# Kernel tuning notes

Measured on AMD Instinct MI355X. Metric: run time of the kernel, lower is better.

## Reference

```python
import jax, jax.numpy as jnp
import numpy as np

HID_X = 64
MLP_RATIO = 4
EPS_NORM = 1e-12  # F.normalize default eps
EPS_RMS = 1e-6


def _l2norm_dim2(w):
    # normalize along dim=-2 (the input-feature axis of each per-sample matrix)
    n = jnp.sqrt(jnp.sum(w * w, axis=-2, keepdims=True))
    return w / jnp.maximum(n, EPS_NORM)


def setup_inputs() -> dict:
    key = jax.random.key(0)
    k1, k2, k3, k4 = jax.random.split(key, 4)
    B, N, D, S = 64, 4096, HID_X, 1024
    total = 3 * D * D * MLP_RATIO
    x = jax.random.normal(k1, (B, N, D), dtype=jnp.float32)
    s = jax.random.normal(k2, (B, S), dtype=jnp.float32)
    W_pg = jax.random.normal(k3, (S, total), dtype=jnp.float32) * 0.02
    b_pg = jax.random.normal(k4, (total,), dtype=jnp.float32) * 0.01
    scale = jnp.ones((D,), dtype=jnp.float32)
    return {"x": x, "s": s, "W_pg": W_pg, "b_pg": b_pg, "scale": scale}


def reference(x, s, W_pg, b_pg, scale):
    B, N, D = x.shape
    H = D * MLP_RATIO
    # hypernetwork: generate per-sample MLP weights
    mlp_params = s @ W_pg + b_pg  # [B, 3*D*H]
    g_p, v_p, f_p = jnp.split(mlp_params, 3, axis=-1)
    fc1_gate = _l2norm_dim2(g_p.reshape(B, D, H))
    fc1_value = _l2norm_dim2(v_p.reshape(B, D, H))
    fc2 = _l2norm_dim2(f_p.reshape(B, H, D))
    # RMSNorm (eps=1e-6)
    rrms = jax.lax.rsqrt(jnp.mean(x * x, axis=-1, keepdims=True) + EPS_RMS)
    xn = x * rrms * scale
    gate = jnp.einsum('bnd,bdh->bnh', xn, fc1_gate)
    value = jnp.einsum('bnd,bdh->bnh', xn, fc1_value)
    h = jax.nn.silu(gate) * value
    out = jnp.einsum('bnh,bhd->bnd', h, fc2) + x
    return out
```

## Files before the change

kernel.cpp:

```cpp
#include <hip/hip_runtime.h>
#include <hip/hip_bf16.h>

#define BB 64
#define NN 4096
#define DD 64
#define HH 256
#define SS 1024
#define TOTAL 49152
#define MAT_ELEMS 16384

typedef __bf16 bf16x8 __attribute__((ext_vector_type(8)));
typedef float  f32x4  __attribute__((ext_vector_type(4)));

__global__ __launch_bounds__(256, 4) void k1_gemm(
    const float* __restrict__ s, const float* __restrict__ W,
    const float* __restrict__ bias, float* __restrict__ params)
{
    const int n0 = blockIdx.x * 64;
    const int t  = threadIdx.x;
    const int tx = t & 15, ty = t >> 4;

    __shared__ float sA[64 * 36];
    __shared__ float sB[32 * 68];

    float acc[4][4] = {};

    for (int k0 = 0; k0 < SS; k0 += 32) {
        #pragma unroll
        for (int i = 0; i < 2; i++) {
            int f4i = t + i * 256;
            int m = f4i >> 3, k4 = f4i & 7;
            float4 v = *(const float4*)&s[m * SS + k0 + k4 * 4];
            *(float4*)&sA[m * 36 + k4 * 4] = v;
        }
        #pragma unroll
        for (int i = 0; i < 2; i++) {
            int f4i = t + i * 256;
            int kk = f4i >> 4, n4 = f4i & 15;
            float4 v = *(const float4*)&W[(size_t)(k0 + kk) * TOTAL + n0 + n4 * 4];
            *(float4*)&sB[kk * 68 + n4 * 4] = v;
        }
        __syncthreads();
        #pragma unroll
        for (int kk = 0; kk < 32; kk++) {
            float4 b = *(const float4*)&sB[kk * 68 + tx * 4];
            float a0 = sA[(ty * 4 + 0) * 36 + kk];
            float a1 = sA[(ty * 4 + 1) * 36 + kk];
            float a2 = sA[(ty * 4 + 2) * 36 + kk];
            float a3 = sA[(ty * 4 + 3) * 36 + kk];
            acc[0][0] += a0 * b.x; acc[0][1] += a0 * b.y; acc[0][2] += a0 * b.z; acc[0][3] += a0 * b.w;
            acc[1][0] += a1 * b.x; acc[1][1] += a1 * b.y; acc[1][2] += a1 * b.z; acc[1][3] += a1 * b.w;
            acc[2][0] += a2 * b.x; acc[2][1] += a2 * b.y; acc[2][2] += a2 * b.z; acc[2][3] += a2 * b.w;
            acc[3][0] += a3 * b.x; acc[3][1] += a3 * b.y; acc[3][2] += a3 * b.z; acc[3][3] += a3 * b.w;
        }
        __syncthreads();
    }

    #pragma unroll
    for (int r = 0; r < 4; r++) {
        int m = ty * 4 + r;
        int n = n0 + tx * 4;
        float4 bv = *(const float4*)&bias[n];
        float4 o;
        o.x = acc[r][0] + bv.x; o.y = acc[r][1] + bv.y;
        o.z = acc[r][2] + bv.z; o.w = acc[r][3] + bv.w;
        *(float4*)&params[(size_t)m * TOTAL + n] = o;
    }
}

__global__ __launch_bounds__(256) void k2_fc1(
    const float* __restrict__ params, __bf16* __restrict__ WgT, __bf16* __restrict__ WvT)
{
    const int b   = blockIdx.x >> 2;
    const int mat = (blockIdx.x >> 1) & 1;
    const int hh  = blockIdx.x & 1;
    const int t   = threadIdx.x;
    __shared__ float sh[64 * 130];
    __shared__ float rnorm[128];

    const float* src = params + (size_t)b * TOTAL + mat * MAT_ELEMS + hh * 128;
    #pragma unroll
    for (int i = 0; i < 32; i++) {
        int idx = t + i * 256;
        int d = idx >> 7, h = idx & 127;
        sh[d * 130 + h] = src[d * 256 + h];
    }
    __syncthreads();
    if (t < 128) {
        float sum = 0.f;
        #pragma unroll
        for (int d = 0; d < 64; d++) {
            float v = sh[d * 130 + t];
            sum += v * v;
        }
        rnorm[t] = 1.0f / fmaxf(sqrtf(sum), 1e-12f);
    }
    __syncthreads();
    __bf16* dst = (mat ? WvT : WgT) + (size_t)b * MAT_ELEMS;
    #pragma unroll
    for (int i = 0; i < 32; i++) {
        int idx = t + i * 256;
        int hl = idx >> 6, d = idx & 63;
        dst[(hh * 128 + hl) * 64 + d] = (__bf16)(sh[d * 130 + hl] * rnorm[hl]);
    }
}

__global__ __launch_bounds__(256) void k2_fc2(
    const float* __restrict__ params, __bf16* __restrict__ WfT)
{
    const int b  = blockIdx.x >> 1;
    const int dh = blockIdx.x & 1;
    const int t  = threadIdx.x;
    __shared__ float sh[256 * 33];
    __shared__ float psum[8 * 32];
    __shared__ float rnorm[32];

    const float* src = params + (size_t)b * TOTAL + 2 * MAT_ELEMS + dh * 32;
    #pragma unroll
    for (int i = 0; i < 32; i++) {
        int idx = t + i * 256;
        int h = idx >> 5, d = idx & 31;
        sh[h * 33 + d] = src[h * 64 + d];
    }
    __syncthreads();
    {
        int d = t & 31, seg = t >> 5;
        float sum = 0.f;
        #pragma unroll
        for (int hi = 0; hi < 32; hi++) {
            float v = sh[(seg * 32 + hi) * 33 + d];
            sum += v * v;
        }
        psum[seg * 32 + d] = sum;
    }
    __syncthreads();
    if (t < 32) {
        float sum = 0.f;
        #pragma unroll
        for (int seg = 0; seg < 8; seg++) sum += psum[seg * 32 + t];
        rnorm[t] = 1.0f / fmaxf(sqrtf(sum), 1e-12f);
    }
    __syncthreads();
    __bf16* dst = WfT + (size_t)b * MAT_ELEMS;
    #pragma unroll
    for (int i = 0; i < 32; i++) {
        int idx = t + i * 256;
        int d = idx >> 8, h = idx & 255;
        dst[(dh * 32 + d) * 256 + h] = (__bf16)(sh[h * 33 + d] * rnorm[d]);
    }
}

__global__ __launch_bounds__(256, 4) void k3_fused(
    const float* __restrict__ x, const float* __restrict__ scale,
    const __bf16* __restrict__ WgT, const __bf16* __restrict__ WvT,
    const __bf16* __restrict__ WfT, float* __restrict__ out)
{
    const int b    = blockIdx.x >> 5;
    const int rb   = blockIdx.x & 31;
    const int t    = threadIdx.x;
    const int w    = t >> 6;
    const int lane = t & 63;
    const int l15  = lane & 15;
    const int quad = lane >> 4;

    __shared__ __bf16 h_sh[4 * 32 * 36];

    const size_t row_base = ((size_t)b * NN + rb * 128) * DD;

    float sc[16];
    *(float4*)&sc[0]  = *(const float4*)&scale[quad * 8];
    *(float4*)&sc[4]  = *(const float4*)&scale[quad * 8 + 4];
    *(float4*)&sc[8]  = *(const float4*)&scale[32 + quad * 8];
    *(float4*)&sc[12] = *(const float4*)&scale[32 + quad * 8 + 4];

    bf16x8 afrag[2][2];
    #pragma unroll
    for (int mt = 0; mt < 2; mt++) {
        int row = w * 32 + mt * 16 + l15;
        const float* xp = &x[row_base + (size_t)row * DD + quad * 8];
        float v[16];
        *(float4*)&v[0]  = *(const float4*)(xp);
        *(float4*)&v[4]  = *(const float4*)(xp + 4);
        *(float4*)&v[8]  = *(const float4*)(xp + 32);
        *(float4*)&v[12] = *(const float4*)(xp + 36);
        float ss = 0.f;
        #pragma unroll
        for (int j = 0; j < 16; j++) ss += v[j] * v[j];
        ss += __shfl_xor(ss, 16, 64);
        ss += __shfl_xor(ss, 32, 64);
        float rr = rsqrtf(ss * (1.0f / 64.0f) + 1e-6f);
        #pragma unroll
        for (int j = 0; j < 8; j++) {
            afrag[mt][0][j] = (__bf16)(v[j] * rr * sc[j]);
            afrag[mt][1][j] = (__bf16)(v[8 + j] * rr * sc[8 + j]);
        }
    }

    f32x4 oacc[2][4] = {};
    const __bf16* wg_b = WgT + (size_t)b * MAT_ELEMS;
    const __bf16* wv_b = WvT + (size_t)b * MAT_ELEMS;
    const __bf16* wf_b = WfT + (size_t)b * MAT_ELEMS;
    __bf16* hbuf = &h_sh[w * 32 * 36];

    for (int np = 0; np < 8; np++) {
        bf16x8 bg[2][2], bv[2][2], bf[4];
        #pragma unroll
        for (int sub = 0; sub < 2; sub++) {
            int nt = np * 2 + sub;
            const __bf16* gp = &wg_b[(nt * 16 + l15) * 64 + quad * 8];
            const __bf16* vp = &wv_b[(nt * 16 + l15) * 64 + quad * 8];
            bg[sub][0] = *(const bf16x8*)(gp);
            bg[sub][1] = *(const bf16x8*)(gp + 32);
            bv[sub][0] = *(const bf16x8*)(vp);
            bv[sub][1] = *(const bf16x8*)(vp + 32);
        }
        #pragma unroll
        for (int dt = 0; dt < 4; dt++)
            bf[dt] = *(const bf16x8*)&wf_b[(dt * 16 + l15) * 256 + np * 32 + quad * 8];

        #pragma unroll
        for (int sub = 0; sub < 2; sub++) {
            #pragma unroll
            for (int mt = 0; mt < 2; mt++) {
                f32x4 g = {0.f, 0.f, 0.f, 0.f}, vv = {0.f, 0.f, 0.f, 0.f};
                g  = __builtin_amdgcn_mfma_f32_16x16x32_bf16(afrag[mt][0], bg[sub][0], g, 0, 0, 0);
                g  = __builtin_amdgcn_mfma_f32_16x16x32_bf16(afrag[mt][1], bg[sub][1], g, 0, 0, 0);
                vv = __builtin_amdgcn_mfma_f32_16x16x32_bf16(afrag[mt][0], bv[sub][0], vv, 0, 0, 0);
                vv = __builtin_amdgcn_mfma_f32_16x16x32_bf16(afrag[mt][1], bv[sub][1], vv, 0, 0, 0);
                #pragma unroll
                for (int r = 0; r < 4; r++) {
                    float gv = g[r];
                    float sig = __builtin_amdgcn_rcpf(1.0f + __expf(-gv));
                    float hval = gv * sig * vv[r];
                    hbuf[(mt * 16 + quad * 4 + r) * 36 + sub * 16 + l15] = (__bf16)hval;
                }
            }
        }
        #pragma unroll
        for (int mt = 0; mt < 2; mt++) {
            bf16x8 ah = *(const bf16x8*)&hbuf[(mt * 16 + l15) * 36 + quad * 8];
            #pragma unroll
            for (int dt = 0; dt < 4; dt++)
                oacc[mt][dt] = __builtin_amdgcn_mfma_f32_16x16x32_bf16(ah, bf[dt], oacc[mt][dt], 0, 0, 0);
        }
    }

    #pragma unroll
    for (int mt = 0; mt < 2; mt++) {
        int r0 = w * 32 + mt * 16 + quad * 4;
        #pragma unroll
        for (int rg = 0; rg < 4; rg++) {
            size_t roff = row_base + (size_t)(r0 + rg) * DD;
            #pragma unroll
            for (int dt = 0; dt < 4; dt++) {
                int col = dt * 16 + l15;
                out[roff + col] = oacc[mt][dt][rg] + x[roff + col];
            }
        }
    }
}

extern "C" void kernel_launch(void* const* d_in, const int* in_sizes, int n_in,
                              void* d_out, int out_size, void* d_ws, size_t ws_size,
                              hipStream_t stream)
{
    const float* x     = (const float*)d_in[0];
    const float* s     = (const float*)d_in[1];
    const float* W_pg  = (const float*)d_in[2];
    const float* b_pg  = (const float*)d_in[3];
    const float* scale = (const float*)d_in[4];
    float* out = (float*)d_out;

    char* ws = (char*)d_ws;
    float*  params = (float*)ws;
    __bf16* WgT    = (__bf16*)(ws + 12582912);
    __bf16* WvT    = (__bf16*)(ws + 14680064);
    __bf16* WfT    = (__bf16*)(ws + 16777216);

    k1_gemm<<<TOTAL / 64, 256, 0, stream>>>(s, W_pg, b_pg, params);
    k2_fc1<<<BB * 4, 256, 0, stream>>>(params, WgT, WvT);
    k2_fc2<<<BB * 2, 256, 0, stream>>>(params, WfT);
    k3_fused<<<BB * 32, 256, 0, stream>>>(x, scale, WgT, WvT, WfT, out);
}
```

Baseline: 457.0 us.

## Prefetch hypernet GEMM tiles into registers and batch fused MLP h stores per half

The hypernetwork GEMM now loads the next k-tile of s and W into registers while the current tile is being computed, so global load latency overlaps the FMA loop. The fused MLP kernel now produces h for four 32-column chunks into a wider per-wave shared buffer, then runs the fc2 MFMAs over all four chunks together, in two halves instead of eight interleaved steps. This is meant to put more independent MFMA and memory work between the h writes and reads. In exchange the fused kernel's LDS grows from about 9 KB to about 35 KB per block, which may reduce occupancy, and the prefetch registers add pressure in the GEMM.

```diff
diff --git a/kernel.cpp b/kernel.cpp
--- a/kernel.cpp
+++ b/kernel.cpp
@@ -25,22 +25,28 @@
 
     float acc[4][4] = {};
 
+    const float* sp0 = &s[(size_t)(t >> 3) * SS + (t & 7) * 4];
+    const float* sp1 = sp0 + (size_t)32 * SS;
+    const float* wp0 = &W[(size_t)(t >> 4) * TOTAL + n0 + (t & 15) * 4];
+    const float* wp1 = wp0 + (size_t)16 * TOTAL;
+
+    float4 pA0 = *(const float4*)(sp0);
+    float4 pA1 = *(const float4*)(sp1);
+    float4 pB0 = *(const float4*)(wp0);
+    float4 pB1 = *(const float4*)(wp1);
+
     for (int k0 = 0; k0 < SS; k0 += 32) {
-        #pragma unroll
-        for (int i = 0; i < 2; i++) {
-            int f4i = t + i * 256;
-            int m = f4i >> 3, k4 = f4i & 7;
-            float4 v = *(const float4*)&s[m * SS + k0 + k4 * 4];
-            *(float4*)&sA[m * 36 + k4 * 4] = v;
-        }
-        #pragma unroll
-        for (int i = 0; i < 2; i++) {
-            int f4i = t + i * 256;
-            int kk = f4i >> 4, n4 = f4i & 15;
-            float4 v = *(const float4*)&W[(size_t)(k0 + kk) * TOTAL + n0 + n4 * 4];
-            *(float4*)&sB[kk * 68 + n4 * 4] = v;
-        }
+        *(float4*)&sA[(t >> 3) * 36 + (t & 7) * 4]        = pA0;
+        *(float4*)&sA[((t >> 3) + 32) * 36 + (t & 7) * 4] = pA1;
+        *(float4*)&sB[(t >> 4) * 68 + (t & 15) * 4]        = pB0;
+        *(float4*)&sB[((t >> 4) + 16) * 68 + (t & 15) * 4] = pB1;
         __syncthreads();
+        if (k0 + 32 < SS) {
+            pA0 = *(const float4*)(sp0 + k0 + 32);
+            pA1 = *(const float4*)(sp1 + k0 + 32);
+            pB0 = *(const float4*)(wp0 + (size_t)(k0 + 32) * TOTAL);
+            pB1 = *(const float4*)(wp1 + (size_t)(k0 + 32) * TOTAL);
+        }
         #pragma unroll
         for (int kk = 0; kk < 32; kk++) {
             float4 b = *(const float4*)&sB[kk * 68 + tx * 4];
@@ -163,7 +169,7 @@
     const int l15  = lane & 15;
     const int quad = lane >> 4;
 
-    __shared__ __bf16 h_sh[4 * 32 * 36];
+    __shared__ __bf16 h_sh[4 * 32 * 136];
 
     const size_t row_base = ((size_t)b * NN + rb * 128) * DD;
 
@@ -200,48 +206,56 @@
     const __bf16* wg_b = WgT + (size_t)b * MAT_ELEMS;
     const __bf16* wv_b = WvT + (size_t)b * MAT_ELEMS;
     const __bf16* wf_b = WfT + (size_t)b * MAT_ELEMS;
-    __bf16* hbuf = &h_sh[w * 32 * 36];
-
-    for (int np = 0; np < 8; np++) {
-        bf16x8 bg[2][2], bv[2][2], bf[4];
-        #pragma unroll
-        for (int sub = 0; sub < 2; sub++) {
-            int nt = np * 2 + sub;
-            const __bf16* gp = &wg_b[(nt * 16 + l15) * 64 + quad * 8];
-            const __bf16* vp = &wv_b[(nt * 16 + l15) * 64 + quad * 8];
-            bg[sub][0] = *(const bf16x8*)(gp);
-            bg[sub][1] = *(const bf16x8*)(gp + 32);
-            bv[sub][0] = *(const bf16x8*)(vp);
-            bv[sub][1] = *(const bf16x8*)(vp + 32);
-        }
-        #pragma unroll
-        for (int dt = 0; dt < 4; dt++)
-            bf[dt] = *(const bf16x8*)&wf_b[(dt * 16 + l15) * 256 + np * 32 + quad * 8];
-
-        #pragma unroll
-        for (int sub = 0; sub < 2; sub++) {
+    __bf16* hbuf = &h_sh[w * 32 * 136];
+
+    for (int half = 0; half < 2; half++) {
+        #pragma unroll
+        for (int npl = 0; npl < 4; npl++) {
+            const int np = half * 4 + npl;
+            bf16x8 bg[2][2], bv[2][2];
+            #pragma unroll
+            for (int sub = 0; sub < 2; sub++) {
+                int nt = np * 2 + sub;
+                const __bf16* gp = &wg_b[(nt * 16 + l15) * 64 + quad * 8];
+                const __bf16* vp = &wv_b[(nt * 16 + l15) * 64 + quad * 8];
+                bg[sub][0] = *(const bf16x8*)(gp);
+                bg[sub][1] = *(const bf16x8*)(gp + 32);
+                bv[sub][0] = *(const bf16x8*)(vp);
+                bv[sub][1] = *(const bf16x8*)(vp + 32);
+            }
+            #pragma unroll
+            for (int sub = 0; sub < 2; sub++) {
+                #pragma unroll
+                for (int mt = 0; mt < 2; mt++) {
+                    f32x4 g = {0.f, 0.f, 0.f, 0.f}, vv = {0.f, 0.f, 0.f, 0.f};
+                    g  = __builtin_amdgcn_mfma_f32_16x16x32_bf16(afrag[mt][0], bg[sub][0], g, 0, 0, 0);
+                    g  = __builtin_amdgcn_mfma_f32_16x16x32_bf16(afrag[mt][1], bg[sub][1], g, 0, 0, 0);
+                    vv = __builtin_amdgcn_mfma_f32_16x16x32_bf16(afrag[mt][0], bv[sub][0], vv, 0, 0, 0);
+                    vv = __builtin_amdgcn_mfma_f32_16x16x32_bf16(afrag[mt][1], bv[sub][1], vv, 0, 0, 0);
+                    #pragma unroll
+                    for (int r = 0; r < 4; r++) {
+                        float gv = g[r];
+                        float sig = __builtin_amdgcn_rcpf(1.0f + __expf(-gv));
+                        float hval = gv * sig * vv[r];
+                        hbuf[(mt * 16 + quad * 4 + r) * 136 + npl * 32 + sub * 16 + l15] = (__bf16)hval;
+                    }
+                }
+            }
+        }
+        #pragma unroll
+        for (int kpl = 0; kpl < 4; kpl++) {
+            const int kp = half * 4 + kpl;
+            bf16x8 bf[4];
+            #pragma unroll
+            for (int dt = 0; dt < 4; dt++)
+                bf[dt] = *(const bf16x8*)&wf_b[(dt * 16 + l15) * 256 + kp * 32 + quad * 8];
             #pragma unroll
             for (int mt = 0; mt < 2; mt++) {
-                f32x4 g = {0.f, 0.f, 0.f, 0.f}, vv = {0.f, 0.f, 0.f, 0.f};
-                g  = __builtin_amdgcn_mfma_f32_16x16x32_bf16(afrag[mt][0], bg[sub][0], g, 0, 0, 0);
-                g  = __builtin_amdgcn_mfma_f32_16x16x32_bf16(afrag[mt][1], bg[sub][1], g, 0, 0, 0);
-                vv = __builtin_amdgcn_mfma_f32_16x16x32_bf16(afrag[mt][0], bv[sub][0], vv, 0, 0, 0);
-                vv = __builtin_amdgcn_mfma_f32_16x16x32_bf16(afrag[mt][1], bv[sub][1], vv, 0, 0, 0);
+                bf16x8 ah = *(const bf16x8*)&hbuf[(mt * 16 + l15) * 136 + kpl * 32 + quad * 8];
                 #pragma unroll
-                for (int r = 0; r < 4; r++) {
-                    float gv = g[r];
-                    float sig = __builtin_amdgcn_rcpf(1.0f + __expf(-gv));
-                    float hval = gv * sig * vv[r];
-                    hbuf[(mt * 16 + quad * 4 + r) * 36 + sub * 16 + l15] = (__bf16)hval;
-                }
-            }
-        }
-        #pragma unroll
-        for (int mt = 0; mt < 2; mt++) {
-            bf16x8 ah = *(const bf16x8*)&hbuf[(mt * 16 + l15) * 36 + quad * 8];
-            #pragma unroll
-            for (int dt = 0; dt < 4; dt++)
-                oacc[mt][dt] = __builtin_amdgcn_mfma_f32_16x16x32_bf16(ah, bf[dt], oacc[mt][dt], 0, 0, 0);
+                for (int dt = 0; dt < 4; dt++)
+                    oacc[mt][dt] = __builtin_amdgcn_mfma_f32_16x16x32_bf16(ah, bf[dt], oacc[mt][dt], 0, 0, 0);
+            }
         }
     }
 
```

After: 440.8 us. 1.04x faster.
